# Optimization experiments

Measured on AMD Instinct MI355X. Metric: run time of the kernel, lower is better.

Reference implementation:

```python
import jax, jax.numpy as jnp
import numpy as np

N = 50000      # nodes
E = 800000     # edges
IN_DIM = 128
HID = 16       # per-head hidden dim (layer1)
HEADS = 8
OUT_DIM = 32   # layer2 output dim (1 head)
NEG_SLOPE = 0.2  # GAT-paper LeakyReLU slope


def _gat_layer(x, W, a_src, a_dst, src, dst, num_nodes):
    """One multi-head GAT layer.
    x: [N, Fin]; W: [Fin, H*D]; a_src/a_dst: [H, D]; src/dst: [E].
    Returns [N, H, D].
    """
    H, D = a_src.shape
    z = (x @ W).reshape(num_nodes, H, D)            # [N, H, D]
    # edge attention logits: attn_fc([z_src || z_dst]) split into two dots
    e_s = jnp.einsum('nhd,hd->nh', z, a_src)        # [N, H]
    e_d = jnp.einsum('nhd,hd->nh', z, a_dst)        # [N, H]
    e = e_s[src] + e_d[dst]                          # [E, H]
    e = jnp.where(e >= 0, e, NEG_SLOPE * e)          # leaky_relu
    # softmax over incoming edges of each destination node
    m = jax.ops.segment_max(e, dst, num_segments=num_nodes)   # [N, H]
    ex = jnp.exp(e - m[dst])                                   # [E, H]
    s = jax.ops.segment_sum(ex, dst, num_segments=num_nodes)  # [N, H]
    alpha = ex / s[dst]                                        # [E, H]
    msg = alpha[:, :, None] * z[src]                            # [E, H, D]
    return jax.ops.segment_sum(msg, dst, num_segments=num_nodes)  # [N, H, D]


def setup_inputs() -> dict:
    key = jax.random.key(0)
    ks = jax.random.split(key, 9)
    h = jax.random.normal(ks[0], (N, IN_DIM), dtype=jnp.float32)
    src = jax.random.randint(ks[1], (E,), 0, N, dtype=jnp.int32)
    dst = jax.random.randint(ks[2], (E,), 0, N, dtype=jnp.int32)
    sc1 = 1.0 / np.sqrt(IN_DIM)
    W1 = jax.random.normal(ks[3], (IN_DIM, HEADS * HID), dtype=jnp.float32) * sc1
    a1_src = jax.random.normal(ks[4], (HEADS, HID), dtype=jnp.float32) * 0.1
    a1_dst = jax.random.normal(ks[5], (HEADS, HID), dtype=jnp.float32) * 0.1
    sc2 = 1.0 / np.sqrt(HEADS * HID)
    W2 = jax.random.normal(ks[6], (HEADS * HID, OUT_DIM), dtype=jnp.float32) * sc2
    a2_src = jax.random.normal(ks[7], (1, OUT_DIM), dtype=jnp.float32) * 0.1
    a2_dst = jax.random.normal(ks[8], (1, OUT_DIM), dtype=jnp.float32) * 0.1
    return {"h": h, "W1": W1, "a1_src": a1_src, "a1_dst": a1_dst,
            "W2": W2, "a2_src": a2_src, "a2_dst": a2_dst,
            "src": src, "dst": dst}


def reference(h, W1, a1_src, a1_dst, W2, a2_src, a2_dst, src, dst):
    # layer1: multi-head, concat heads -> [N, HEADS*HID]
    h1 = _gat_layer(h, W1, a1_src, a1_dst, src, dst, N).reshape(N, HEADS * HID)
    h1 = jax.nn.elu(h1)
    # layer2: single head -> [N, OUT_DIM]
    out = _gat_layer(h1, W2, a2_src, a2_dst, src, dst, N).reshape(N, OUT_DIM)
    return out
```

## Files before the change

kernel.cpp:

```cpp
#include <hip/hip_runtime.h>
#include <hip/hip_fp16.h>
#include <math.h>

#define NN 50000
#define EE 800000
#define FIN 128
#define F1  128
#define NH  8
#define DH  16
#define F2  32
#define SLOPE 0.2f
#define LOG2E 1.44269504f

#define EB 4096
#define NBLK ((EE + EB - 1) / EB)
#define HB 2048
#define NHBLK ((EE + HB - 1) / HB)
#define BK  391
#define SEGCAP 4096
#define W1XN 144
#define W2XN 34
#define PREPB ((W1XN * 128 + W2XN * 128 + 255) / 256)
#define GEMM1B ((NN + 63) / 64)
#define ATT1B  (((NN + 63) / 64) * 8)
#define GEMM2B ((NN + 63) / 64)
#define CHUNK 1280
#define ATT2B ((NN + 31) / 32)
#define CHUNK2 1024

typedef _Float16 f16x8 __attribute__((ext_vector_type(8)));
typedef float    f32x4 __attribute__((ext_vector_type(4)));

__global__ __launch_bounds__(256) void k1_hist_prep(const int* __restrict__ dst,
        const float* __restrict__ W1, const float* __restrict__ W2,
        const float* __restrict__ a1s, const float* __restrict__ a1d,
        const float* __restrict__ a2s, const float* __restrict__ a2d,
        __half* __restrict__ wt1, __half* __restrict__ wt2, int* __restrict__ hist) {
    int tid = threadIdx.x;
    if (blockIdx.x < NHBLK) {
        __shared__ int lc[BK];
        for (int i = tid; i < BK; i += 256) lc[i] = 0;
        __syncthreads();
        int base = blockIdx.x * HB;
        int end = base + HB; if (end > EE) end = EE;
        for (int i = base + tid; i < end; i += 256)
            atomicAdd(&lc[dst[i] >> 7], 1);
        __syncthreads();
        for (int i = tid; i < BK; i += 256)
            if (lc[i]) atomicAdd(&hist[i], lc[i]);
    } else {
        int gidx = (blockIdx.x - NHBLK) * 256 + tid;
        if (gidx < W1XN * 128) {
            int n = gidx >> 7, k = gidx & 127;
            float v;
            if (n < 128) {
                v = W1[k * F1 + n];
            } else if (n < 136) {
                int c = n - 128; float s = 0.f;
                #pragma unroll
                for (int d = 0; d < 16; ++d) s += W1[k * F1 + c * 16 + d] * a1s[c * 16 + d];
                v = s * LOG2E;
            } else {
                int c = n - 136; float s = 0.f;
                #pragma unroll
                for (int d = 0; d < 16; ++d) s += W1[k * F1 + c * 16 + d] * a1d[c * 16 + d];
                v = s * LOG2E;
            }
            wt1[gidx] = __float2half(v);
        } else {
            int t2 = gidx - W1XN * 128;
            if (t2 < W2XN * 128) {
                int n = t2 >> 7, k = t2 & 127;
                float v;
                if (n < 32) {
                    v = W2[k * F2 + n];
                } else {
                    const float* av = (n == 32) ? a2s : a2d;
                    float s = 0.f;
                    #pragma unroll
                    for (int d = 0; d < 32; ++d) s += W2[k * F2 + d] * av[d];
                    v = s * LOG2E;
                }
                wt2[t2] = __float2half(v);
            }
        }
    }
}

extern __shared__ char smem_k2[];
__global__ __launch_bounds__(256) void k2_split_gemm1(const int* __restrict__ src,
        const int* __restrict__ dst, const int* __restrict__ hist, int* __restrict__ cursor,
        unsigned int* __restrict__ sorted,
        const float* __restrict__ h, const __half* __restrict__ wt1,
        __half* __restrict__ z1s, float* __restrict__ es1x, float* __restrict__ ed1x) {
    int tid = threadIdx.x;
    if (blockIdx.x < NBLK) {
        unsigned int*   recs = (unsigned int*)smem_k2;
        unsigned short* rbk  = (unsigned short*)(smem_k2 + 16384);
        int* lc    = (int*)(smem_k2 + 24576);
        int* lofs  = (int*)(smem_k2 + 26624);
        int* lcur  = (int*)(smem_k2 + 28672);
        int* delta = (int*)(smem_k2 + 30720);
        int* bscan = (int*)(smem_k2 + 32768);
        int* sh    = (int*)(smem_k2 + 34816);
        for (int i = tid; i < 512; i += 256) lc[i] = 0;
        __syncthreads();
        int base = blockIdx.x * EB;
        int cnt = EE - base; if (cnt > EB) cnt = EB;
        unsigned int myrec[16];
        #pragma unroll
        for (int k = 0; k < 16; ++k) {
            int i = base + tid + k * 256;
            myrec[k] = 0xFFFFFFFFu;
            if (i - base < cnt) {
                unsigned int d = (unsigned int)dst[i];
                myrec[k] = (d << 16) | (unsigned int)src[i];
                atomicAdd(&lc[d >> 7], 1);
            }
        }
        __syncthreads();
        int a0 = lc[2 * tid], a1 = lc[2 * tid + 1];
        int tsum = a0 + a1;
        sh[tid] = tsum;
        __syncthreads();
        for (int off = 1; off < 256; off <<= 1) {
            int t = (tid >= off) ? sh[tid - off] : 0;
            __syncthreads(); sh[tid] += t; __syncthreads();
        }
        int ex = sh[tid] - tsum;
        lofs[2 * tid] = ex;
        lofs[2 * tid + 1] = ex + a0;
        __syncthreads();
        int h0 = hist[2 * tid], h1 = hist[2 * tid + 1];
        int hsum = h0 + h1;
        sh[tid] = hsum;
        __syncthreads();
        for (int off = 1; off < 256; off <<= 1) {
            int t = (tid >= off) ? sh[tid - off] : 0;
            __syncthreads(); sh[tid] += t; __syncthreads();
        }
        int hex = sh[tid] - hsum;
        bscan[2 * tid] = hex;
        bscan[2 * tid + 1] = hex + h0;
        __syncthreads();
        for (int b = tid; b < BK; b += 256) {
            int c = lc[b];
            lcur[b] = lofs[b];
            if (c) {
                int g = atomicAdd(&cursor[b], c);
                delta[b] = bscan[b] + g - lofs[b];
            }
        }
        __syncthreads();
        #pragma unroll
        for (int k = 0; k < 16; ++k) {
            if (myrec[k] != 0xFFFFFFFFu) {
                int b = (int)(myrec[k] >> 23);
                int pos = atomicAdd(&lcur[b], 1);
                recs[pos] = myrec[k];
                rbk[pos] = (unsigned short)b;
            }
        }
        __syncthreads();
        for (int s = tid; s < cnt; s += 256)
            sorted[s + delta[rbk[s]]] = recs[s];
    } else {
        __half* hs  = (__half*)smem_k2;
        __half* wls = (__half*)(smem_k2 + 17408);
        for (int c = tid; c < W1XN * 16; c += 256) {
            int row = c >> 4, ch = c & 15;
            *(float4*)&wls[row * 136 + ch * 8] = *(const float4*)&wt1[row * 128 + ch * 8];
        }
        int rowBase = (blockIdx.x - NBLK) * 64;
        for (int idx4 = tid; idx4 < 64 * 32; idx4 += 256) {
            int r = idx4 >> 5, cc = (idx4 & 31) * 4;
            int n = rowBase + r;
            float4 v = (n < NN) ? *(const float4*)&h[(size_t)n * FIN + cc] : make_float4(0, 0, 0, 0);
            union { __half2 h2[2]; int2 i; } u;
            u.h2[0] = __floats2half2_rn(v.x, v.y);
            u.h2[1] = __floats2half2_rn(v.z, v.w);
            *(int2*)&hs[r * 136 + cc] = u.i;
        }
        __syncthreads();
        int l = tid & 63, w = tid >> 6;
        int q = l >> 4, cl = l & 15;
        int m0 = w * 16;
        f32x4 acc[9];
        #pragma unroll
        for (int t = 0; t < 9; ++t) acc[t] = (f32x4){0.f, 0.f, 0.f, 0.f};
        const __half* ap = &hs[(m0 + cl) * 136 + q * 8];
        const __half* bp = &wls[cl * 136 + q * 8];
        #pragma unroll
        for (int k0 = 0; k0 < 128; k0 += 32) {
            f16x8 af = *(const f16x8*)(ap + k0);
            #pragma unroll
            for (int t = 0; t < 9; ++t) {
                f16x8 bf = *(const f16x8*)(bp + t * 16 * 136 + k0);
                acc[t] = __builtin_amdgcn_mfma_f32_16x16x32_f16(af, bf, acc[t], 0, 0, 0);
            }
        }
        #pragma unroll
        for (int t = 0; t < 8; ++t) {
            #pragma unroll
            for (int reg = 0; reg < 4; ++reg) {
                int row = rowBase + m0 + q * 4 + reg;
                if (row < NN)
                    z1s[(size_t)t * (NN * 16) + (size_t)row * 16 + cl] = __float2half(acc[t][reg]);
            }
        }
        #pragma unroll
        for (int reg = 0; reg < 4; ++reg) {
            int row = rowBase + m0 + q * 4 + reg;
            if (row < NN) {
                float v = acc[8][reg];
                if (cl < 8) es1x[row * NH + cl] = v;
                else        ed1x[row * NH + (cl - 8)] = v;
            }
        }
    }
}

__global__ __launch_bounds__(256) void csrbuild_kernel(const int* __restrict__ hist,
        const unsigned int* __restrict__ sorted, unsigned short* __restrict__ csr,
        const float* __restrict__ es1x, const float* __restrict__ ed1x,
        float* __restrict__ w1p, int* __restrict__ row_ptr) {
    __shared__ unsigned int recs[SEGCAP];
    __shared__ unsigned short csr_sh[SEGCAP];
    __shared__ unsigned char dst_sh[SEGCAP];
    __shared__ float ed_sh[128 * NH];
    __shared__ int ncnt[128], ncur[128];
    __shared__ int sh[256];
    __shared__ int bscan[512];
    int b = blockIdx.x;
    int tid = threadIdx.x;
    int h0 = hist[2 * tid], h1 = hist[2 * tid + 1];
    int hsum = h0 + h1;
    sh[tid] = hsum;
    if (tid < 128) ncnt[tid] = 0;
    for (int idx = tid; idx < 128 * NH; idx += 256) {
        int node = b * 128 + (idx >> 3);
        ed_sh[idx] = (node < NN) ? ed1x[node * NH + (idx & 7)] : 0.f;
    }
    __syncthreads();
    for (int off = 1; off < 256; off <<= 1) {
        int t = (tid >= off) ? sh[tid - off] : 0;
        __syncthreads(); sh[tid] += t; __syncthreads();
    }
    int hex = sh[tid] - hsum;
    bscan[2 * tid] = hex;
    bscan[2 * tid + 1] = hex + h0;
    __syncthreads();
    int s0 = bscan[b], s1 = bscan[b + 1];
    int cnt = s1 - s0; if (cnt > SEGCAP) cnt = SEGCAP;
    for (int i = tid; i < cnt; i += 256) {
        unsigned int r = sorted[s0 + i];
        recs[i] = r;
        atomicAdd(&ncnt[(r >> 16) & 127], 1);
    }
    __syncthreads();
    int v = (tid < 128) ? ncnt[tid] : 0;
    sh[tid] = v;
    __syncthreads();
    for (int off = 1; off < 256; off <<= 1) {
        int t = (tid >= off) ? sh[tid - off] : 0;
        __syncthreads(); sh[tid] += t; __syncthreads();
    }
    int ex = sh[tid] - v;
    if (tid < 128) {
        ncur[tid] = ex;
        int node = b * 128 + tid;
        if (node < NN) row_ptr[node] = s0 + ex;
    }
    if (b == BK - 1 && tid == 0) row_ptr[NN] = EE;
    __syncthreads();
    for (int i = tid; i < cnt; i += 256) {
        unsigned int r = recs[i];
        int local = (r >> 16) & 127;
        int p = atomicAdd(&ncur[local], 1);
        csr_sh[p] = (unsigned short)(r & 0xFFFFu);
        dst_sh[p] = (unsigned char)local;
    }
    __syncthreads();
    for (int i = tid; i < cnt; i += 256) {
        unsigned short sv = csr_sh[i];
        unsigned char lv = dst_sh[i];
        csr[s0 + i] = sv;
        float4 ea = *(const float4*)&es1x[(size_t)sv * NH];
        float4 eb = *(const float4*)&es1x[(size_t)sv * NH + 4];
        float es8[8] = {ea.x, ea.y, ea.z, ea.w, eb.x, eb.y, eb.z, eb.w};
        const float* edp = &ed_sh[(int)lv * NH];
        #pragma unroll
        for (int hh = 0; hh < 8; ++hh) {
            float e = es8[hh] + edp[hh];
            e = e >= 0.f ? e : SLOPE * e;
            w1p[(size_t)hh * EE + s0 + i] = exp2f(e);
        }
    }
}

__global__ __launch_bounds__(128, 8) void attn1_slice_kernel(const int* __restrict__ row_ptr,
        const unsigned short* __restrict__ csr, const __half* __restrict__ z1s,
        const float* __restrict__ w1p, __half* __restrict__ h1s) {
    __shared__ unsigned short csr_sh[CHUNK];
    __shared__ float w_sh[CHUNK];
    int hl = blockIdx.x & 7;
    int tile = blockIdx.x >> 3;
    int nodeBase = tile * 64;
    int tid = threadIdx.x;
    int n = nodeBase + (tid >> 1);
    int j = tid & 1;
    const __half* zp = z1s + (size_t)hl * (NN * 16) + j * 8;
    const float* wp = w1p + (size_t)hl * EE;
    int tBeg = row_ptr[nodeBase];
    int nEnd = nodeBase + 64; if (nEnd > NN) nEnd = NN;
    int tEnd = row_ptr[nEnd];
    int b0 = 0, b1 = -1;
    if (n < NN) { b0 = row_ptr[n]; b1 = row_ptr[n + 1]; }
    float acc[8] = {0.f, 0.f, 0.f, 0.f, 0.f, 0.f, 0.f, 0.f};
    float ws = 0.f;
    for (int c0 = tBeg; c0 < tEnd; c0 += CHUNK) {
        int c1 = c0 + CHUNK; if (c1 > tEnd) c1 = tEnd;
        for (int i = c0 + tid; i < c1; i += 128) {
            csr_sh[i - c0] = csr[i];
            w_sh[i - c0] = wp[i];
        }
        __syncthreads();
        int lo = b0 > c0 ? b0 : c0;
        int hi = b1 < c1 ? b1 : c1;
        int i = lo;
        for (; i + 4 <= hi; i += 4) {
            int r = i - c0;
            int s0 = csr_sh[r], s1 = csr_sh[r + 1], s2 = csr_sh[r + 2], s3 = csr_sh[r + 3];
            float w0 = w_sh[r], w1 = w_sh[r + 1], w2 = w_sh[r + 2], w3 = w_sh[r + 3];
            union { float4 f; __half2 h2[4]; } u0, u1, u2, u3;
            u0.f = *(const float4*)&zp[(size_t)s0 * 16];
            u1.f = *(const float4*)&zp[(size_t)s1 * 16];
            u2.f = *(const float4*)&zp[(size_t)s2 * 16];
            u3.f = *(const float4*)&zp[(size_t)s3 * 16];
            ws += (w0 + w1) + (w2 + w3);
            #pragma unroll
            for (int t = 0; t < 4; ++t) {
                float2 v0 = __half22float2(u0.h2[t]);
                float2 v1 = __half22float2(u1.h2[t]);
                float2 v2 = __half22float2(u2.h2[t]);
                float2 v3 = __half22float2(u3.h2[t]);
                acc[2*t]   = fmaf(w0, v0.x, fmaf(w1, v1.x, fmaf(w2, v2.x, fmaf(w3, v3.x, acc[2*t]))));
                acc[2*t+1] = fmaf(w0, v0.y, fmaf(w1, v1.y, fmaf(w2, v2.y, fmaf(w3, v3.y, acc[2*t+1]))));
            }
        }
        for (; i < hi; ++i) {
            int r = i - c0;
            int s = csr_sh[r];
            float wv = w_sh[r];
            ws += wv;
            union { float4 f; __half2 h2[4]; } u;
            u.f = *(const float4*)&zp[(size_t)s * 16];
            #pragma unroll
            for (int t = 0; t < 4; ++t) {
                float2 v = __half22float2(u.h2[t]);
                acc[2*t]   = fmaf(wv, v.x, acc[2*t]);
                acc[2*t+1] = fmaf(wv, v.y, acc[2*t+1]);
            }
        }
        __syncthreads();
    }
    if (n < NN) {
        float rs = ws > 0.f ? 1.0f / ws : 0.f;
        union { float4 f; __half2 h2[4]; } p;
        #pragma unroll
        for (int t = 0; t < 4; ++t) {
            float x0 = acc[2*t] * rs, x1 = acc[2*t+1] * rs;
            x0 = x0 > 0.f ? x0 : __expf(x0) - 1.0f;
            x1 = x1 > 0.f ? x1 : __expf(x1) - 1.0f;
            p.h2[t] = __floats2half2_rn(x0, x1);
        }
        *(float4*)&h1s[(size_t)hl * (NN * 16) + (size_t)n * 16 + j * 8] = p.f;
    }
}

__global__ __launch_bounds__(256) void gemm2_kernel(const __half* __restrict__ h1s,
        const __half* __restrict__ wt2,
        __half* __restrict__ z2h, float* __restrict__ es2x, float* __restrict__ ed2x) {
    __shared__ alignas(16) __half hs[64 * 136];
    __shared__ alignas(16) __half wls[48 * 136];
    int tid = threadIdx.x;
    for (int c = tid; c < 48 * 16; c += 256) {
        int row = c >> 4, ch = c & 15;
        float4 v = make_float4(0.f, 0.f, 0.f, 0.f);
        if (row < W2XN) v = *(const float4*)&wt2[row * 128 + ch * 8];
        *(float4*)&wls[row * 136 + ch * 8] = v;
    }
    int rowBase = blockIdx.x * 64;
    for (int idx = tid; idx < 1024; idx += 256) {
        int j2 = idx & 1, nl = (idx >> 1) & 63, pl = idx >> 7;
        int n = rowBase + nl;
        float4 v = (n < NN) ? *(const float4*)&h1s[(size_t)pl * (NN * 16) + (size_t)n * 16 + j2 * 8]
                            : make_float4(0, 0, 0, 0);
        *(float4*)&hs[nl * 136 + pl * 16 + j2 * 8] = v;
    }
    __syncthreads();
    int l = tid & 63, w = tid >> 6;
    int q = l >> 4, cl = l & 15;
    int m0 = w * 16;
    f32x4 acc2[3];
    acc2[0] = (f32x4){0.f, 0.f, 0.f, 0.f};
    acc2[1] = (f32x4){0.f, 0.f, 0.f, 0.f};
    acc2[2] = (f32x4){0.f, 0.f, 0.f, 0.f};
    const __half* ap = &hs[(m0 + cl) * 136 + q * 8];
    const __half* bp = &wls[cl * 136 + q * 8];
    #pragma unroll
    for (int k0 = 0; k0 < 128; k0 += 32) {
        f16x8 af = *(const f16x8*)(ap + k0);
        #pragma unroll
        for (int t = 0; t < 3; ++t) {
            f16x8 bf = *(const f16x8*)(bp + t * 16 * 136 + k0);
            acc2[t] = __builtin_amdgcn_mfma_f32_16x16x32_f16(af, bf, acc2[t], 0, 0, 0);
        }
    }
    #pragma unroll
    for (int reg = 0; reg < 4; ++reg) {
        int row = rowBase + m0 + q * 4 + reg;
        if (row < NN) {
            z2h[(size_t)row * F2 + cl]      = __float2half(acc2[0][reg]);
            z2h[(size_t)row * F2 + 16 + cl] = __float2half(acc2[1][reg]);
            if (cl == 0)      es2x[row] = acc2[2][reg];
            else if (cl == 1) ed2x[row] = acc2[2][reg];
        }
    }
}

__global__ __launch_bounds__(128, 8) void attn2_kernel(const int* __restrict__ row_ptr,
        const unsigned short* __restrict__ csr, const __half* __restrict__ z2h,
        const float* __restrict__ es, const float* __restrict__ ed,
        float* __restrict__ out) {
    __shared__ unsigned short csr_sh[CHUNK2];
    __shared__ float es_sh[CHUNK2];
    int nodeBase = blockIdx.x * 32;
    int tid = threadIdx.x;
    int j = tid & 3;
    int n = nodeBase + (tid >> 2);
    int tBeg = row_ptr[nodeBase];
    int nEnd = nodeBase + 32; if (nEnd > NN) nEnd = NN;
    int tEnd = row_ptr[nEnd];
    int b0 = 0, b1 = -1;
    float edn = 0.f;
    if (n < NN) { b0 = row_ptr[n]; b1 = row_ptr[n + 1]; edn = ed[n]; }
    float acc[8] = {0.f, 0.f, 0.f, 0.f, 0.f, 0.f, 0.f, 0.f};
    float ws = 0.f;
    for (int c0 = tBeg; c0 < tEnd; c0 += CHUNK2) {
        int c1 = c0 + CHUNK2; if (c1 > tEnd) c1 = tEnd;
        for (int i = c0 + tid; i < c1; i += 128) {
            unsigned short s = csr[i];
            csr_sh[i - c0] = s;
            es_sh[i - c0] = es[s];
        }
        __syncthreads();
        int lo = b0 > c0 ? b0 : c0;
        int hi = b1 < c1 ? b1 : c1;
        int i = lo;
        for (; i + 4 <= hi; i += 4) {
            int r = i - c0;
            int s0 = csr_sh[r], s1 = csr_sh[r + 1], s2 = csr_sh[r + 2], s3 = csr_sh[r + 3];
            float e0 = es_sh[r] + edn;
            float e1 = es_sh[r + 1] + edn;
            float e2 = es_sh[r + 2] + edn;
            float e3 = es_sh[r + 3] + edn;
            union { float4 f; __half2 h2[4]; } u0, u1, u2, u3;
            u0.f = *(const float4*)&z2h[(size_t)s0 * F2 + j * 8];
            u1.f = *(const float4*)&z2h[(size_t)s1 * F2 + j * 8];
            u2.f = *(const float4*)&z2h[(size_t)s2 * F2 + j * 8];
            u3.f = *(const float4*)&z2h[(size_t)s3 * F2 + j * 8];
            float w0 = exp2f(e0 >= 0.f ? e0 : SLOPE * e0);
            float w1 = exp2f(e1 >= 0.f ? e1 : SLOPE * e1);
            float w2 = exp2f(e2 >= 0.f ? e2 : SLOPE * e2);
            float w3 = exp2f(e3 >= 0.f ? e3 : SLOPE * e3);
            ws += (w0 + w1) + (w2 + w3);
            #pragma unroll
            for (int t = 0; t < 4; ++t) {
                float2 v0 = __half22float2(u0.h2[t]);
                float2 v1 = __half22float2(u1.h2[t]);
                float2 v2 = __half22float2(u2.h2[t]);
                float2 v3 = __half22float2(u3.h2[t]);
                acc[2*t]   = fmaf(w0, v0.x, fmaf(w1, v1.x, fmaf(w2, v2.x, fmaf(w3, v3.x, acc[2*t]))));
                acc[2*t+1] = fmaf(w0, v0.y, fmaf(w1, v1.y, fmaf(w2, v2.y, fmaf(w3, v3.y, acc[2*t+1]))));
            }
        }
        for (; i < hi; ++i) {
            int r = i - c0;
            int s = csr_sh[r];
            float e = es_sh[r] + edn;
            float wv = exp2f(e >= 0.f ? e : SLOPE * e);
            ws += wv;
            union { float4 f; __half2 h2[4]; } u;
            u.f = *(const float4*)&z2h[(size_t)s * F2 + j * 8];
            #pragma unroll
            for (int t = 0; t < 4; ++t) {
                float2 v = __half22float2(u.h2[t]);
                acc[2*t]   = fmaf(wv, v.x, acc[2*t]);
                acc[2*t+1] = fmaf(wv, v.y, acc[2*t+1]);
            }
        }
        __syncthreads();
    }
    if (n < NN) {
        float rs = ws > 0.f ? 1.0f / ws : 0.f;
        *(float4*)&out[(size_t)n * F2 + j * 8] =
            make_float4(acc[0]*rs, acc[1]*rs, acc[2]*rs, acc[3]*rs);
        *(float4*)&out[(size_t)n * F2 + j * 8 + 4] =
            make_float4(acc[4]*rs, acc[5]*rs, acc[6]*rs, acc[7]*rs);
    }
}

extern "C" void kernel_launch(void* const* d_in, const int* in_sizes, int n_in,
                              void* d_out, int out_size, void* d_ws, size_t ws_size,
                              hipStream_t stream) {
    const float* h   = (const float*)d_in[0];
    const float* W1  = (const float*)d_in[1];
    const float* a1s = (const float*)d_in[2];
    const float* a1d = (const float*)d_in[3];
    const float* W2  = (const float*)d_in[4];
    const float* a2s = (const float*)d_in[5];
    const float* a2d = (const float*)d_in[6];
    const int*   src = (const int*)d_in[7];
    const int*   dst = (const int*)d_in[8];
    float* out = (float*)d_out;

    int* ip      = (int*)d_ws;
    int* hist    = ip;
    int* cursor  = hist + 512;
    int* row_ptr = cursor + 512;
    unsigned int* sorted = (unsigned int*)(row_ptr + NN + 8);
    unsigned short* csr16 = (unsigned short*)(sorted + EE);
    float* es1x = (float*)(csr16 + EE);
    float* ed1x = es1x + (size_t)NN * NH;
    float* es2x = ed1x + (size_t)NN * NH;
    float* ed2x = es2x + NN;
    __half* z1s = (__half*)(ed2x + NN);
    __half* z2h = z1s + (size_t)NN * F1;
    __half* wt1 = z2h + (size_t)NN * F2;
    __half* wt2 = wt1 + W1XN * 128;
    __half* h1s = wt2 + W2XN * 128;
    float* w1p  = (float*)(h1s + (size_t)NN * F1);

    hipMemsetAsync(hist, 0, 1024 * sizeof(int), stream);

    k1_hist_prep<<<NHBLK + PREPB, 256, 0, stream>>>(dst, W1, W2, a1s, a1d, a2s, a2d,
                                                    wt1, wt2, hist);
    k2_split_gemm1<<<NBLK + GEMM1B, 256, 56576, stream>>>(src, dst, hist, cursor, sorted,
                                                          h, wt1, z1s, es1x, ed1x);
    csrbuild_kernel<<<BK, 256, 0, stream>>>(hist, sorted, csr16, es1x, ed1x, w1p, row_ptr);
    attn1_slice_kernel<<<ATT1B, 128, 0, stream>>>(row_ptr, csr16, z1s, w1p, h1s);
    gemm2_kernel<<<GEMM2B, 256, 0, stream>>>(h1s, wt2, z2h, es2x, ed2x);
    attn2_kernel<<<ATT2B, 128, 0, stream>>>(row_ptr, csr16, z2h, es2x, ed2x, out);
}
```

Baseline: 190.6 us.

## Compute layer-1 edge attention weights inside attn1 instead of materializing them in CSR build

The CSR build kernel no longer computes per-edge, per-head exp2(leaky_relu(es+ed)) weights into a 25.6 MB w1p buffer. The attn1 kernel now gathers head-major source logits (es1h) per edge into shared memory and computes the weights on the fly, adding the destination logit held in a register. The GEMM1 epilogue writes es/ed in head-major layout so each head slice is contiguous. This removes a large write and read of per-edge weights, at the cost of an extra random gather of es per edge per head and recomputing exp2 in the aggregation loop.

```diff
diff --git a/kernel.cpp b/kernel.cpp
--- a/kernel.cpp
+++ b/kernel.cpp
@@ -92,7 +92,7 @@
         const int* __restrict__ dst, const int* __restrict__ hist, int* __restrict__ cursor,
         unsigned int* __restrict__ sorted,
         const float* __restrict__ h, const __half* __restrict__ wt1,
-        __half* __restrict__ z1s, float* __restrict__ es1x, float* __restrict__ ed1x) {
+        __half* __restrict__ z1s, float* __restrict__ es1h, float* __restrict__ ed1h) {
     int tid = threadIdx.x;
     if (blockIdx.x < NBLK) {
         unsigned int*   recs = (unsigned int*)smem_k2;
@@ -213,8 +213,8 @@
             int row = rowBase + m0 + q * 4 + reg;
             if (row < NN) {
                 float v = acc[8][reg];
-                if (cl < 8) es1x[row * NH + cl] = v;
-                else        ed1x[row * NH + (cl - 8)] = v;
+                if (cl < 8) es1h[(size_t)cl * NN + row] = v;
+                else        ed1h[(size_t)(cl - 8) * NN + row] = v;
             }
         }
     }
@@ -222,12 +222,9 @@
 
 __global__ __launch_bounds__(256) void csrbuild_kernel(const int* __restrict__ hist,
         const unsigned int* __restrict__ sorted, unsigned short* __restrict__ csr,
-        const float* __restrict__ es1x, const float* __restrict__ ed1x,
-        float* __restrict__ w1p, int* __restrict__ row_ptr) {
+        int* __restrict__ row_ptr) {
     __shared__ unsigned int recs[SEGCAP];
     __shared__ unsigned short csr_sh[SEGCAP];
-    __shared__ unsigned char dst_sh[SEGCAP];
-    __shared__ float ed_sh[128 * NH];
     __shared__ int ncnt[128], ncur[128];
     __shared__ int sh[256];
     __shared__ int bscan[512];
@@ -237,10 +234,6 @@
     int hsum = h0 + h1;
     sh[tid] = hsum;
     if (tid < 128) ncnt[tid] = 0;
-    for (int idx = tid; idx < 128 * NH; idx += 256) {
-        int node = b * 128 + (idx >> 3);
-        ed_sh[idx] = (node < NN) ? ed1x[node * NH + (idx & 7)] : 0.f;
-    }
     __syncthreads();
     for (int off = 1; off < 256; off <<= 1) {
         int t = (tid >= off) ? sh[tid - off] : 0;
@@ -278,31 +271,18 @@
         int local = (r >> 16) & 127;
         int p = atomicAdd(&ncur[local], 1);
         csr_sh[p] = (unsigned short)(r & 0xFFFFu);
-        dst_sh[p] = (unsigned char)local;
-    }
-    __syncthreads();
-    for (int i = tid; i < cnt; i += 256) {
-        unsigned short sv = csr_sh[i];
-        unsigned char lv = dst_sh[i];
-        csr[s0 + i] = sv;
-        float4 ea = *(const float4*)&es1x[(size_t)sv * NH];
-        float4 eb = *(const float4*)&es1x[(size_t)sv * NH + 4];
-        float es8[8] = {ea.x, ea.y, ea.z, ea.w, eb.x, eb.y, eb.z, eb.w};
-        const float* edp = &ed_sh[(int)lv * NH];
-        #pragma unroll
-        for (int hh = 0; hh < 8; ++hh) {
-            float e = es8[hh] + edp[hh];
-            e = e >= 0.f ? e : SLOPE * e;
-            w1p[(size_t)hh * EE + s0 + i] = exp2f(e);
-        }
-    }
+    }
+    __syncthreads();
+    for (int i = tid; i < cnt; i += 256)
+        csr[s0 + i] = csr_sh[i];
 }
 
 __global__ __launch_bounds__(128, 8) void attn1_slice_kernel(const int* __restrict__ row_ptr,
         const unsigned short* __restrict__ csr, const __half* __restrict__ z1s,
-        const float* __restrict__ w1p, __half* __restrict__ h1s) {
+        const float* __restrict__ es1h, const float* __restrict__ ed1h,
+        __half* __restrict__ h1s) {
     __shared__ unsigned short csr_sh[CHUNK];
-    __shared__ float w_sh[CHUNK];
+    __shared__ float es_sh[CHUNK];
     int hl = blockIdx.x & 7;
     int tile = blockIdx.x >> 3;
     int nodeBase = tile * 64;
@@ -310,19 +290,21 @@
     int n = nodeBase + (tid >> 1);
     int j = tid & 1;
     const __half* zp = z1s + (size_t)hl * (NN * 16) + j * 8;
-    const float* wp = w1p + (size_t)hl * EE;
+    const float* esp = es1h + (size_t)hl * NN;
     int tBeg = row_ptr[nodeBase];
     int nEnd = nodeBase + 64; if (nEnd > NN) nEnd = NN;
     int tEnd = row_ptr[nEnd];
     int b0 = 0, b1 = -1;
-    if (n < NN) { b0 = row_ptr[n]; b1 = row_ptr[n + 1]; }
+    float edn = 0.f;
+    if (n < NN) { b0 = row_ptr[n]; b1 = row_ptr[n + 1]; edn = ed1h[(size_t)hl * NN + n]; }
     float acc[8] = {0.f, 0.f, 0.f, 0.f, 0.f, 0.f, 0.f, 0.f};
     float ws = 0.f;
     for (int c0 = tBeg; c0 < tEnd; c0 += CHUNK) {
         int c1 = c0 + CHUNK; if (c1 > tEnd) c1 = tEnd;
         for (int i = c0 + tid; i < c1; i += 128) {
-            csr_sh[i - c0] = csr[i];
-            w_sh[i - c0] = wp[i];
+            unsigned short s = csr[i];
+            csr_sh[i - c0] = s;
+            es_sh[i - c0] = esp[s];
         }
         __syncthreads();
         int lo = b0 > c0 ? b0 : c0;
@@ -331,12 +313,19 @@
         for (; i + 4 <= hi; i += 4) {
             int r = i - c0;
             int s0 = csr_sh[r], s1 = csr_sh[r + 1], s2 = csr_sh[r + 2], s3 = csr_sh[r + 3];
-            float w0 = w_sh[r], w1 = w_sh[r + 1], w2 = w_sh[r + 2], w3 = w_sh[r + 3];
+            float e0 = es_sh[r] + edn;
+            float e1 = es_sh[r + 1] + edn;
+            float e2 = es_sh[r + 2] + edn;
+            float e3 = es_sh[r + 3] + edn;
             union { float4 f; __half2 h2[4]; } u0, u1, u2, u3;
             u0.f = *(const float4*)&zp[(size_t)s0 * 16];
             u1.f = *(const float4*)&zp[(size_t)s1 * 16];
             u2.f = *(const float4*)&zp[(size_t)s2 * 16];
             u3.f = *(const float4*)&zp[(size_t)s3 * 16];
+            float w0 = exp2f(e0 >= 0.f ? e0 : SLOPE * e0);
+            float w1 = exp2f(e1 >= 0.f ? e1 : SLOPE * e1);
+            float w2 = exp2f(e2 >= 0.f ? e2 : SLOPE * e2);
+            float w3 = exp2f(e3 >= 0.f ? e3 : SLOPE * e3);
             ws += (w0 + w1) + (w2 + w3);
             #pragma unroll
             for (int t = 0; t < 4; ++t) {
@@ -351,7 +340,8 @@
         for (; i < hi; ++i) {
             int r = i - c0;
             int s = csr_sh[r];
-            float wv = w_sh[r];
+            float e = es_sh[r] + edn;
+            float wv = exp2f(e >= 0.f ? e : SLOPE * e);
             ws += wv;
             union { float4 f; __half2 h2[4]; } u;
             u.f = *(const float4*)&zp[(size_t)s * 16];
@@ -531,25 +521,24 @@
     int* row_ptr = cursor + 512;
     unsigned int* sorted = (unsigned int*)(row_ptr + NN + 8);
     unsigned short* csr16 = (unsigned short*)(sorted + EE);
-    float* es1x = (float*)(csr16 + EE);
-    float* ed1x = es1x + (size_t)NN * NH;
-    float* es2x = ed1x + (size_t)NN * NH;
+    float* es1h = (float*)(csr16 + EE);
+    float* ed1h = es1h + (size_t)NN * NH;
+    float* es2x = ed1h + (size_t)NN * NH;
     float* ed2x = es2x + NN;
     __half* z1s = (__half*)(ed2x + NN);
     __half* z2h = z1s + (size_t)NN * F1;
     __half* wt1 = z2h + (size_t)NN * F2;
     __half* wt2 = wt1 + W1XN * 128;
     __half* h1s = wt2 + W2XN * 128;
-    float* w1p  = (float*)(h1s + (size_t)NN * F1);
 
     hipMemsetAsync(hist, 0, 1024 * sizeof(int), stream);
 
     k1_hist_prep<<<NHBLK + PREPB, 256, 0, stream>>>(dst, W1, W2, a1s, a1d, a2s, a2d,
                                                     wt1, wt2, hist);
     k2_split_gemm1<<<NBLK + GEMM1B, 256, 56576, stream>>>(src, dst, hist, cursor, sorted,
-                                                          h, wt1, z1s, es1x, ed1x);
-    csrbuild_kernel<<<BK, 256, 0, stream>>>(hist, sorted, csr16, es1x, ed1x, w1p, row_ptr);
-    attn1_slice_kernel<<<ATT1B, 128, 0, stream>>>(row_ptr, csr16, z1s, w1p, h1s);
+                                                          h, wt1, z1s, es1h, ed1h);
+    csrbuild_kernel<<<BK, 256, 0, stream>>>(hist, sorted, csr16, row_ptr);
+    attn1_slice_kernel<<<ATT1B, 128, 0, stream>>>(row_ptr, csr16, z1s, es1h, ed1h, h1s);
     gemm2_kernel<<<GEMM2B, 256, 0, stream>>>(h1s, wt2, z2h, es2x, ed2x);
     attn2_kernel<<<ATT2B, 128, 0, stream>>>(row_ptr, csr16, z2h, es2x, ed2x, out);
 }
```

Result: slower. 201.1 us (+5.5%).
